# Kernel tuning notes

Hardware: AMD Instinct MI355X
Metric: run time of the kernel (lower is better)

Reference implementation:

```python
import jax, jax.numpy as jnp
import numpy as np

H, KV, D = 12, 2, 128        # q heads, kv heads, head_dim
HID = 1536
B, S = 4, 2048               # equal-length packed sequences
T = B * S
EPS = 1e-6
ROPE_THETA = 10000.0


def _rms_norm(x, w):
    # RMSNorm over last dim in fp32, as in Qwen3RMSNorm
    xf = x.astype(jnp.float32)
    var = jnp.mean(xf * xf, axis=-1, keepdims=True)
    return (w * (xf * jax.lax.rsqrt(var + EPS))).astype(x.dtype)


def _apply_rope(x, cos, sin):
    # x: [T, h, D]; cos/sin: [T, D/2] -> expand over heads
    half = cos.shape[-1]
    x1, x2 = x[..., :half], x[..., half:2 * half]
    c = cos[:, None, :]
    s = sin[:, None, :]
    return jnp.concatenate([x1 * c - x2 * s, x1 * s + x2 * c], axis=-1)


def setup_inputs() -> dict:
    key = jax.random.key(0)
    ks = jax.random.split(key, 8)
    hidden_states = jax.random.normal(ks[0], (T, HID), dtype=jnp.float32)
    # real RoPE tables over per-sequence positions
    inv_freq = 1.0 / (ROPE_THETA ** (np.arange(0, D, 2, dtype=np.float32) / D))  # [D/2]
    pos = np.tile(np.arange(S, dtype=np.float32), B)                              # [T]
    ang = pos[:, None] * inv_freq[None, :]
    cos = jnp.asarray(np.cos(ang), dtype=jnp.float32)
    sin = jnp.asarray(np.sin(ang), dtype=jnp.float32)
    sc = 0.02
    Wq = jax.random.normal(ks[1], (HID, H * D), dtype=jnp.float32) * sc
    Wk = jax.random.normal(ks[2], (HID, KV * D), dtype=jnp.float32) * sc
    Wv = jax.random.normal(ks[3], (HID, KV * D), dtype=jnp.float32) * sc
    Wo = jax.random.normal(ks[4], (H * D, HID), dtype=jnp.float32) * sc
    q_norm_w = jnp.ones((D,), dtype=jnp.float32)
    k_norm_w = jnp.ones((D,), dtype=jnp.float32)
    cu_seqlens = jnp.arange(B + 1, dtype=jnp.int32) * S
    return {"hidden_states": hidden_states, "cos": cos, "sin": sin,
            "Wq": Wq, "Wk": Wk, "Wv": Wv, "Wo": Wo,
            "q_norm_w": q_norm_w, "k_norm_w": k_norm_w,
            "cu_seqlens": cu_seqlens}


def reference(hidden_states, cos, sin, Wq, Wk, Wv, Wo, q_norm_w, k_norm_w, cu_seqlens):
    # QKV projections on packed tokens
    q = (hidden_states @ Wq).reshape(T, H, D)
    k = (hidden_states @ Wk).reshape(T, KV, D)
    v = (hidden_states @ Wv).reshape(T, KV, D)
    # Qwen3 per-head QK RMSNorm, then RoPE
    q = _apply_rope(_rms_norm(q, q_norm_w), cos, sin)
    k = _apply_rope(_rms_norm(k, k_norm_w), cos, sin)
    # equal-length sequences: unpack to [B, h, S, D] (block-diagonal varlen attn)
    qb = q.reshape(B, S, H, D).transpose(0, 2, 1, 3)
    kb = k.reshape(B, S, KV, D).transpose(0, 2, 1, 3)
    vb = v.reshape(B, S, KV, D).transpose(0, 2, 1, 3)
    # GQA: repeat kv heads
    rep = H // KV
    kb = jnp.repeat(kb, rep, axis=1)
    vb = jnp.repeat(vb, rep, axis=1)
    scale = D ** -0.5
    scores = jnp.einsum('bhqd,bhkd->bhqk', qb, kb) * scale
    causal = jnp.tril(jnp.ones((S, S), dtype=bool))
    scores = jnp.where(causal[None, None], scores, jnp.finfo(scores.dtype).min)
    attn = jax.nn.softmax(scores, axis=-1)
    out = jnp.einsum('bhqk,bhkd->bhqd', attn, vb)       # [B,H,S,D]
    out = out.transpose(0, 2, 1, 3).reshape(T, H * D)   # repack
    return out @ Wo
```

## Files before the change

### kernel.cpp

```cpp
#include <hip/hip_runtime.h>
#include <hip/hip_bf16.h>
#include <stdint.h>

#define H_   12
#define KV_  2
#define D_   128
#define HID_ 1536
#define B_   4
#define S_   2048
#define T_   (B_*S_)

typedef __attribute__((ext_vector_type(8))) short  bf16x8;
typedef __attribute__((ext_vector_type(4))) float  f32x4;

__device__ __forceinline__ ushort f2bf(float f) {
  union { float f; uint32_t u; } v; v.f = f;
  uint32_t u = v.u;
  return (ushort)((u + 0x7fffu + ((u >> 16) & 1u)) >> 16);
}
__device__ __forceinline__ float bf2f(ushort u) {
  union { uint32_t u; float f; } v; v.u = ((uint32_t)u) << 16;
  return v.f;
}
__device__ __forceinline__ uint32_t cvtpk_bf16(float lo, float hi) {
  uint32_t r;
  asm("v_cvt_pk_bf16_f32 %0, %1, %2" : "=v"(r) : "v"(lo), "v"(hi));
  return r;
}

__device__ __forceinline__ void gload_lds16(const void* g, void* l) {
  __builtin_amdgcn_global_load_lds(
      (const __attribute__((address_space(1))) uint32_t*)g,
      (__attribute__((address_space(3))) uint32_t*)l, 16, 0, 0);
}

__global__ __launch_bounds__(256) void cvt_f32_bf16(const float* __restrict__ in,
                                                    ushort* __restrict__ out, int n) {
  int i = (blockIdx.x * 256 + threadIdx.x) * 4;
  if (i + 3 < n) {
    float4 v = *(const float4*)&in[i];
    ushort4 o;
    o.x = f2bf(v.x); o.y = f2bf(v.y); o.z = f2bf(v.z); o.w = f2bf(v.w);
    *(ushort4*)&out[i] = o;
  }
}

__global__ __launch_bounds__(256) void transpose_cvt2(const float* __restrict__ W0,
                                                      ushort* __restrict__ Wt0,
                                                      const float* __restrict__ W1,
                                                      ushort* __restrict__ Wt1,
                                                      int K, int N) {
  __shared__ float tile[32][33];
  const float* W  = blockIdx.z ? W1  : W0;
  ushort*      Wt = blockIdx.z ? Wt1 : Wt0;
  int k0 = blockIdx.x * 32, n0 = blockIdx.y * 32;
  int tx = threadIdx.x & 31, ty = threadIdx.x >> 5;
#pragma unroll
  for (int i = 0; i < 32; i += 8)
    tile[ty + i][tx] = W[(long)(k0 + ty + i) * N + n0 + tx];
  __syncthreads();
#pragma unroll
  for (int i = 0; i < 32; i += 8)
    Wt[(long)(n0 + ty + i) * K + k0 + tx] = f2bf(tile[tx][ty + i]);
}

template <int OUT_F32>
__global__ __launch_bounds__(256, 2) void gemm_bt(const ushort* __restrict__ A,
                                                  const ushort* __restrict__ Bt,
                                                  void* __restrict__ Cv,
                                                  int M, int N, int K, int lda) {
  __shared__ ushort lA[128 * 32];
  __shared__ ushort lB[128 * 32];
  const int tid = threadIdx.x;
  const int lane = tid & 63, w = tid >> 6;
  const int wr = w >> 1, wc = w & 1;
  const int l15 = lane & 15, lh = lane >> 4;
  const long m0 = (long)blockIdx.x * 128, n0 = (long)blockIdx.y * 128;
  const ushort* Ab = A + m0 * lda;
  const ushort* Bb = Bt + n0 * K;
  const int sr = tid >> 2;
  const int sc = (tid & 3) * 8;
  const int ldsoff = w * 512;
  f32x4 acc[4][4] = {};

  for (int k0 = 0; k0 < K; k0 += 32) {
#pragma unroll
    for (int it = 0; it < 2; ++it) {
      gload_lds16(Ab + (long)(it * 64 + sr) * lda + k0 + sc, &lA[it * 2048 + ldsoff]);
      gload_lds16(Bb + (long)(it * 64 + sr) * K + k0 + sc, &lB[it * 2048 + ldsoff]);
    }
    __syncthreads();
    bf16x8 af[4], bfr[4];
    const int ra = (wr * 64 + l15) * 32 + lh * 8;
    const int rb = (wc * 64 + l15) * 32 + lh * 8;
#pragma unroll
    for (int i = 0; i < 4; ++i) {
      af[i]  = *(const bf16x8*)&lA[ra + i * 16 * 32];
      bfr[i] = *(const bf16x8*)&lB[rb + i * 16 * 32];
    }
#pragma unroll
    for (int i = 0; i < 4; ++i)
#pragma unroll
      for (int j = 0; j < 4; ++j)
        acc[i][j] = __builtin_amdgcn_mfma_f32_16x16x32_bf16(af[i], bfr[j], acc[i][j], 0, 0, 0);
    __syncthreads();
  }
#pragma unroll
  for (int i = 0; i < 4; ++i) {
#pragma unroll
    for (int q = 0; q < 4; ++q) {
      long row = m0 + wr * 64 + i * 16 + lh * 4 + q;
#pragma unroll
      for (int j = 0; j < 4; ++j) {
        long col = n0 + wc * 64 + j * 16 + l15;
        float v = acc[i][j][q];
        if (OUT_F32) ((float*)Cv)[row * N + col] = v;
        else         ((ushort*)Cv)[row * N + col] = f2bf(v);
      }
    }
  }
}

template <int OUT_F32>
__global__ __launch_bounds__(512) void gemm256(const ushort* __restrict__ A,
                                               const ushort* __restrict__ Bt,
                                               void* __restrict__ Cv,
                                               int M, int N, int K, int lda) {
  __shared__ ushort lA[2][256 * 64];
  __shared__ ushort lB[2][256 * 64];
  const int tid = threadIdx.x, lane = tid & 63;
  const int w = tid >> 6;
  const int l15 = lane & 15, lh = lane >> 4;
  const int wr = w >> 2, wc = w & 3;
  const long m0 = (long)blockIdx.x * 256, n0 = (long)blockIdx.y * 256;
  const ushort* Ab = A + m0 * lda;
  const ushort* Bb = Bt + n0 * K;
  const int swz = (l15 & 7) << 4;

  f32x4 acc[8][4] = {};
  const int NT = K / 64;

#define STAGE256(KT, PB) do {                                                      \
  const int k0s = (KT) * 64;                                                       \
  _Pragma("unroll") for (int it = 0; it < 4; ++it) {                               \
    int ch = it * 512 + tid; int r = ch >> 3, s = ch & 7;                          \
    int cb = it * 512 + (tid & 448);                                               \
    gload_lds16(Ab + (long)r * lda + k0s + ((s ^ (r & 7)) * 8), &lA[PB][cb * 8]);  \
  }                                                                                \
  _Pragma("unroll") for (int it = 0; it < 4; ++it) {                               \
    int ch = it * 512 + tid; int r = ch >> 3, s = ch & 7;                          \
    int cb = it * 512 + (tid & 448);                                               \
    gload_lds16(Bb + (long)r * K + k0s + ((s ^ (r & 7)) * 8), &lB[PB][cb * 8]);    \
  }                                                                                \
} while (0)

  STAGE256(0, 0);
  __syncthreads();
  int p = 0;
  for (int kt = 0; kt < NT; ++kt) {
    if (kt + 1 < NT) STAGE256(kt + 1, p ^ 1);
    const char* cA = (const char*)&lA[p][0];
    const char* cB = (const char*)&lB[p][0];
    bf16x8 bf[4][2];
#pragma unroll
    for (int fj = 0; fj < 4; ++fj)
#pragma unroll
      for (int kk = 0; kk < 2; ++kk)
        bf[fj][kk] = *(const bf16x8*)(cB + (wc * 64 + fj * 16 + l15) * 128 + ((kk * 64 + lh * 16) ^ swz));
    __builtin_amdgcn_s_setprio(1);
#pragma unroll
    for (int fi = 0; fi < 8; ++fi) {
      const int ra = (wr * 128 + fi * 16 + l15) * 128;
      bf16x8 af0 = *(const bf16x8*)(cA + ra + ((lh * 16) ^ swz));
      bf16x8 af1 = *(const bf16x8*)(cA + ra + ((64 + lh * 16) ^ swz));
#pragma unroll
      for (int fj = 0; fj < 4; ++fj) {
        acc[fi][fj] = __builtin_amdgcn_mfma_f32_16x16x32_bf16(af0, bf[fj][0], acc[fi][fj], 0, 0, 0);
        acc[fi][fj] = __builtin_amdgcn_mfma_f32_16x16x32_bf16(af1, bf[fj][1], acc[fi][fj], 0, 0, 0);
      }
    }
    __builtin_amdgcn_s_setprio(0);
    __syncthreads();
    p ^= 1;
  }
#undef STAGE256
#pragma unroll
  for (int fi = 0; fi < 8; ++fi) {
#pragma unroll
    for (int q = 0; q < 4; ++q) {
      long row = m0 + wr * 128 + fi * 16 + lh * 4 + q;
#pragma unroll
      for (int fj = 0; fj < 4; ++fj) {
        long col = n0 + wc * 64 + fj * 16 + l15;
        float v = acc[fi][fj][q];
        if (OUT_F32) ((float*)Cv)[row * N + col] = v;
        else         ((ushort*)Cv)[row * N + col] = f2bf(v);
      }
    }
  }
}

template <int NH>
__global__ __launch_bounds__(256) void normrope(const ushort* __restrict__ X,
                                                int xstride,
                                                const float* __restrict__ w,
                                                const float* __restrict__ cosb,
                                                const float* __restrict__ sinb,
                                                ushort* __restrict__ Y,
                                                float scale) {
  int wid = (int)((blockIdx.x * 256 + threadIdx.x) >> 6);
  int lane = threadIdx.x & 63;
  if (wid >= T_ * NH) return;
  int t = wid / NH, h = wid % NH;
  const ushort* xr = X + (long)t * xstride + h * 128;
  float x1 = bf2f(xr[lane]);
  float x2 = bf2f(xr[lane + 64]);
  float ss = x1 * x1 + x2 * x2;
#pragma unroll
  for (int off = 32; off; off >>= 1) ss += __shfl_xor(ss, off);
  float r = rsqrtf(ss * (1.0f / 128.0f) + 1e-6f);
  float y1 = x1 * r * w[lane] * scale;
  float y2 = x2 * r * w[lane + 64] * scale;
  float c = cosb[(long)t * 64 + lane], s = sinb[(long)t * 64 + lane];
  float o1 = y1 * c - y2 * s;
  float o2 = y1 * s + y2 * c;
  int b = t / S_, sq = t % S_;
  ushort* yr = Y + ((long)(b * NH + h) * S_ + sq) * 128;
  yr[lane]      = f2bf(o1);
  yr[lane + 64] = f2bf(o2);
}

__global__ __launch_bounds__(256) void vtrans(const ushort* __restrict__ V, int vstride, int voff,
                                              ushort* __restrict__ Vt) {
  __shared__ ushort tile[32][33];
  int s0 = blockIdx.x * 32, d0 = blockIdx.y * 32;
  int bk = blockIdx.z;
  int b = bk / KV_, g = bk % KV_;
  int tx = threadIdx.x & 31, ty = threadIdx.x >> 5;
#pragma unroll
  for (int i = 0; i < 32; i += 8)
    tile[ty + i][tx] = V[(long)(b * S_ + s0 + ty + i) * vstride + voff + g * 128 + d0 + tx];
  __syncthreads();
#pragma unroll
  for (int i = 0; i < 32; i += 8)
    Vt[(long)(bk * 128 + d0 + ty + i) * S_ + s0 + tx] = tile[tx][ty + i];
}

__global__ __launch_bounds__(256, 2) void attn(ushort* __restrict__ QKV,
                                               const ushort* __restrict__ Ka,
                                               const ushort* __restrict__ Vt,
                                               const float* __restrict__ qnw,
                                               const float* __restrict__ cosb,
                                               const float* __restrict__ sinb) {
  __shared__ ushort lK[64 * 128];
  __shared__ ushort lV[128 * 64];
  __shared__ ushort lP[4 * 32 * 32];
  const int tid = threadIdx.x, lane = tid & 63, w = tid >> 6;
  const int l15 = lane & 15, lh = lane >> 4;
  char* cK = (char*)lK;
  char* cV = (char*)lV;
  char* cP = (char*)lP + w * 2048;
  const int swzK = l15 << 4;
  const int swzV = (l15 & 7) << 4;
  const int swzP = (l15 & 3) << 4;
  const float SCL = 0.08838834764831845f * 1.44269504088896f;
  const float M0  = 17.0f;

  const int qt = 15 - (int)(blockIdx.x / 48);
  const int bh = blockIdx.x % 48;
  const int b = bh / H_, h = bh % H_, g = h / (H_ / KV_);
  const int q0 = qt * 128;
  const ushort* Kb = Ka + (long)(b * KV_ + g) * S_ * 128;
  const ushort* Vb = Vt + (long)(b * KV_ + g) * 128 * S_;

  bf16x8 qf[2][4];
#pragma unroll
  for (int m = 0; m < 2; ++m) {
    const long tt = (long)b * S_ + q0 + w * 32 + m * 16 + l15;
    const ushort* xr = QKV + tt * 2048 + h * 128;
    bf16x8 raw[4];
#pragma unroll
    for (int kd = 0; kd < 4; ++kd)
      raw[kd] = *(const bf16x8*)&xr[kd * 32 + lh * 8];
    float ss = 0.f;
#pragma unroll
    for (int kd = 0; kd < 4; ++kd)
#pragma unroll
      for (int e = 0; e < 8; ++e) {
        float v = bf2f((ushort)raw[kd][e]);
        ss += v * v;
      }
    ss += __shfl_xor(ss, 16);
    ss += __shfl_xor(ss, 32);
    const float rn = rsqrtf(ss * (1.0f / 128.0f) + 1e-6f) * SCL;
    const float* cR = cosb + tt * 64;
    const float* sR = sinb + tt * 64;
#pragma unroll
    for (int kp = 0; kp < 2; ++kp) {
      bf16x8 qlo, qhi;
#pragma unroll
      for (int e = 0; e < 8; ++e) {
        const int ci = kp * 32 + lh * 8 + e;
        float c = cR[ci], s = sR[ci];
        float y1 = bf2f((ushort)raw[kp][e])     * rn * qnw[ci];
        float y2 = bf2f((ushort)raw[kp + 2][e]) * rn * qnw[64 + ci];
        qlo[e] = (short)f2bf(y1 * c - y2 * s);
        qhi[e] = (short)f2bf(y1 * s + y2 * c);
      }
      qf[m][kp]     = qlo;
      qf[m][kp + 2] = qhi;
    }
  }

  f32x4 o[2][8] = {};
  float lr[2] = {0.f, 0.f};
  const int nt = 2 * qt + 2;

  bf16x8 kreg[4], vreg[4];
#define LDTILE(K0) do { \
  _Pragma("unroll") for (int it = 0; it < 4; ++it) \
    kreg[it] = *(const bf16x8*)&Kb[(long)((K0) + it * 16 + (tid >> 4)) * 128 + (tid & 15) * 8]; \
  _Pragma("unroll") for (int it = 0; it < 4; ++it) \
    vreg[it] = *(const bf16x8*)&Vb[(long)(it * 32 + (tid >> 3)) * S_ + (K0) + (tid & 7) * 8]; \
} while (0)

  LDTILE(0);
  for (int t = 0; t < nt; ++t) {
    const int k0 = t * 64;
    __syncthreads();
#pragma unroll
    for (int it = 0; it < 4; ++it) {
      int r = it * 16 + (tid >> 4);
      *(bf16x8*)(cK + r * 256 + (((tid & 15) * 16) ^ (((tid >> 4) & 15) << 4))) = kreg[it];
    }
#pragma unroll
    for (int it = 0; it < 4; ++it) {
      int r = it * 32 + (tid >> 3);
      *(bf16x8*)(cV + r * 128 + (((tid & 7) * 16) ^ ((r & 7) << 4))) = vreg[it];
    }
    __syncthreads();
    if (t + 1 < nt) LDTILE(k0 + 64);

    if (k0 <= q0 + w * 32 + 31) {
      f32x4 sfr[2][4] = {};
      __builtin_amdgcn_s_setprio(1);
#pragma unroll
      for (int kd = 0; kd < 4; ++kd) {
        bf16x8 kf[4];
#pragma unroll
        for (int n = 0; n < 4; ++n)
          kf[n] = *(const bf16x8*)(cK + (n * 16 + l15) * 256 + ((kd * 64 + lh * 16) ^ swzK));
#pragma unroll
        for (int m = 0; m < 2; ++m)
#pragma unroll
          for (int n = 0; n < 4; ++n)
            sfr[m][n] = __builtin_amdgcn_mfma_f32_16x16x32_bf16(kf[n], qf[m][kd], sfr[m][n], 0, 0, 0);
      }
      __builtin_amdgcn_s_setprio(0);
      const bool boundary = (k0 + 63 > q0 + w * 32);
      if (boundary) {
#pragma unroll
        for (int m = 0; m < 2; ++m) {
          const int rowm = q0 + w * 32 + m * 16 + l15;
#pragma unroll
          for (int n = 0; n < 4; ++n) {
            int kb = k0 + n * 16 + lh * 4;
#pragma unroll
            for (int qr = 0; qr < 4; ++qr)
              if (kb + qr > rowm) sfr[m][n][qr] = -INFINITY;
          }
        }
      }
#pragma unroll
      for (int m = 0; m < 2; ++m) {
#pragma unroll
        for (int n = 0; n < 4; ++n) {
          float p0 = exp2f(sfr[m][n][0] - M0);
          float p1 = exp2f(sfr[m][n][1] - M0);
          float p2 = exp2f(sfr[m][n][2] - M0);
          float p3 = exp2f(sfr[m][n][3] - M0);
          sfr[m][n][0] = p0; sfr[m][n][1] = p1; sfr[m][n][2] = p2; sfr[m][n][3] = p3;
          lr[m] += (p0 + p1) + (p2 + p3);
        }
      }
#pragma unroll
      for (int kf2 = 0; kf2 < 2; ++kf2) {
#pragma unroll
        for (int m = 0; m < 2; ++m)
#pragma unroll
          for (int nl = 0; nl < 2; ++nl) {
            const int n = kf2 * 2 + nl;
            uint2 pk;
            pk.x = cvtpk_bf16(sfr[m][n][0], sfr[m][n][1]);
            pk.y = cvtpk_bf16(sfr[m][n][2], sfr[m][n][3]);
            *(uint2*)(cP + (m * 16 + l15) * 64 + ((nl * 32 + lh * 8) ^ swzP)) = pk;
          }
        const int cb = (lh * 16) ^ swzP;
        bf16x8 pf0 = *(const bf16x8*)(cP + l15 * 64 + cb);
        bf16x8 pf1 = *(const bf16x8*)(cP + (16 + l15) * 64 + cb);
        const int cv = (kf2 * 64 + lh * 16);
        __builtin_amdgcn_s_setprio(1);
#pragma unroll
        for (int dblk = 0; dblk < 8; ++dblk) {
          bf16x8 vf = *(const bf16x8*)(cV + (dblk * 16 + l15) * 128 + (cv ^ swzV));
          o[0][dblk] = __builtin_amdgcn_mfma_f32_16x16x32_bf16(pf0, vf, o[0][dblk], 0, 0, 0);
          o[1][dblk] = __builtin_amdgcn_mfma_f32_16x16x32_bf16(pf1, vf, o[1][dblk], 0, 0, 0);
        }
        __builtin_amdgcn_s_setprio(0);
      }
    }
  }
#undef LDTILE
#pragma unroll
  for (int m = 0; m < 2; ++m) {
    lr[m] += __shfl_xor(lr[m], 16);
    lr[m] += __shfl_xor(lr[m], 32);
    float inv = 1.f / lr[m];
#pragma unroll
    for (int qr = 0; qr < 4; ++qr) {
      float iv = __shfl(inv, lh * 4 + qr);
      long trow = (long)b * S_ + q0 + w * 32 + m * 16 + lh * 4 + qr;
#pragma unroll
      for (int dblk = 0; dblk < 8; ++dblk)
        QKV[trow * 2048 + h * 128 + dblk * 16 + l15] = f2bf(o[m][dblk][qr] * iv);
    }
  }
}

extern "C" void kernel_launch(void* const* d_in, const int* in_sizes, int n_in,
                              void* d_out, int out_size, void* d_ws, size_t ws_size,
                              hipStream_t stream) {
  const float* hs   = (const float*)d_in[0];
  const float* cosb = (const float*)d_in[1];
  const float* sinb = (const float*)d_in[2];
  const float* Wq   = (const float*)d_in[3];
  const float* Wk   = (const float*)d_in[4];
  const float* Wv   = (const float*)d_in[5];
  const float* Wo   = (const float*)d_in[6];
  const float* qw   = (const float*)d_in[7];
  const float* kw   = (const float*)d_in[8];
  (void)in_sizes; (void)n_in; (void)out_size; (void)ws_size;

  char* ws = (char*)d_ws;
  size_t off = 0;
  auto alloc = [&](size_t bytes) {
    void* p = ws + off;
    off += (bytes + 255) & ~(size_t)255;
    return p;
  };
  ushort* Xb  = (ushort*)alloc((size_t)T_ * HID_ * 2);
  ushort* Wqt = (ushort*)alloc((size_t)HID_ * HID_ * 2);
  ushort* Wkt = (ushort*)alloc((size_t)256 * HID_ * 2);
  ushort* Wvt = (ushort*)alloc((size_t)256 * HID_ * 2);
  ushort* Wot = (ushort*)alloc((size_t)HID_ * HID_ * 2);
  ushort* qkv = (ushort*)alloc((size_t)T_ * 2048 * 2);
  ushort* ka  = (ushort*)alloc((size_t)T_ * 256 * 2);
  ushort* vt  = (ushort*)alloc((size_t)T_ * 256 * 2);

  cvt_f32_bf16<<<(T_ * HID_ / 4 + 255) / 256, 256, 0, stream>>>(hs, Xb, T_ * HID_);
  transpose_cvt2<<<dim3(HID_ / 32, HID_ / 32, 2), 256, 0, stream>>>(Wq, Wqt, Wo, Wot, HID_, HID_);
  transpose_cvt2<<<dim3(HID_ / 32, 256 / 32, 2), 256, 0, stream>>>(Wk, Wkt, Wv, Wvt, HID_, 256);

  gemm256<0><<<dim3(T_ / 256, 2048 / 256), 512, 0, stream>>>(Xb, Wqt, qkv, T_, 2048, HID_, HID_);

  normrope<KV_><<<(T_ * KV_ + 3) / 4, 256, 0, stream>>>(qkv + 1536, 2048, kw, cosb, sinb, ka, 1.0f);
  vtrans<<<dim3(S_ / 32, 128 / 32, B_ * KV_), 256, 0, stream>>>(qkv, 2048, 1792, vt);

  attn<<<768, 256, 0, stream>>>(qkv, ka, vt, qw, cosb, sinb);

  gemm_bt<1><<<dim3(T_ / 128, 1536 / 128), 256, 0, stream>>>(qkv, Wot, (float*)d_out, T_, 1536, HID_, 2048);
}
```

Before: 215.9 us.

## Split longest causal attention q-tiles across two blocks with finalize merge

The four longest query tiles (qt 12-15) are split along the KV dimension into two halves, each run by its own block, with a custom schedule order that interleaves split and unsplit tiles to balance load. Split blocks write unnormalized fp32 partial outputs and row sums to scratch (reusing the Xb buffer), and a new finalize kernel sums them and normalizes into QKV. This targets the tail imbalance of causal attention, at the cost of extra scratch traffic and one more kernel launch. The merge depends on the fixed max M0 shared across halves, so no max rescaling is needed.

Measured after the change: 225.0 us. +4.2%, slower.

```diff
diff --git a/kernel.cpp b/kernel.cpp
--- a/kernel.cpp
+++ b/kernel.cpp
@@ -246,12 +246,17 @@
     Vt[(long)(bk * 128 + d0 + ty + i) * S_ + s0 + tx] = tile[tx][ty + i];
 }
 
+__device__ const signed char DQT[20] = {11,10,9,8,7,15,15,14,14,6,13,13,12,12,5,4,3,2,1,0};
+__device__ const signed char DHF[20] = {-1,-1,-1,-1,-1, 0, 1, 0, 1,-1, 0, 1, 0, 1,-1,-1,-1,-1,-1,-1};
+
 __global__ __launch_bounds__(256, 2) void attn(ushort* __restrict__ QKV,
                                                const ushort* __restrict__ Ka,
                                                const ushort* __restrict__ Vt,
                                                const float* __restrict__ qnw,
                                                const float* __restrict__ cosb,
-                                               const float* __restrict__ sinb) {
+                                               const float* __restrict__ sinb,
+                                               float* __restrict__ scO,
+                                               float* __restrict__ scL) {
   __shared__ ushort lK[64 * 128];
   __shared__ ushort lV[128 * 64];
   __shared__ ushort lP[4 * 32 * 32];
@@ -266,10 +271,15 @@
   const float SCL = 0.08838834764831845f * 1.44269504088896f;
   const float M0  = 17.0f;
 
-  const int qt = 15 - (int)(blockIdx.x / 48);
+  const int u  = (int)(blockIdx.x / 48);
   const int bh = blockIdx.x % 48;
+  const int qt = DQT[u];
+  const int hf = DHF[u];
   const int b = bh / H_, h = bh % H_, g = h / (H_ / KV_);
   const int q0 = qt * 128;
+  const int t0 = (hf == 1) ? (qt + 1) : 0;
+  const int t1 = (hf == 0) ? (qt + 1) : (2 * qt + 2);
+  const bool split = (hf >= 0);
   const ushort* Kb = Ka + (long)(b * KV_ + g) * S_ * 128;
   const ushort* Vb = Vt + (long)(b * KV_ + g) * 128 * S_;
 
@@ -314,7 +324,6 @@
 
   f32x4 o[2][8] = {};
   float lr[2] = {0.f, 0.f};
-  const int nt = 2 * qt + 2;
 
   bf16x8 kreg[4], vreg[4];
 #define LDTILE(K0) do { \
@@ -324,8 +333,8 @@
     vreg[it] = *(const bf16x8*)&Vb[(long)(it * 32 + (tid >> 3)) * S_ + (K0) + (tid & 7) * 8]; \
 } while (0)
 
-  LDTILE(0);
-  for (int t = 0; t < nt; ++t) {
+  LDTILE(t0 * 64);
+  for (int t = t0; t < t1; ++t) {
     const int k0 = t * 64;
     __syncthreads();
 #pragma unroll
@@ -339,7 +348,7 @@
       *(bf16x8*)(cV + r * 128 + (((tid & 7) * 16) ^ ((r & 7) << 4))) = vreg[it];
     }
     __syncthreads();
-    if (t + 1 < nt) LDTILE(k0 + 64);
+    if (t + 1 < t1) LDTILE((t + 1) * 64);
 
     if (k0 <= q0 + w * 32 + 31) {
       f32x4 sfr[2][4] = {};
@@ -415,15 +424,63 @@
   for (int m = 0; m < 2; ++m) {
     lr[m] += __shfl_xor(lr[m], 16);
     lr[m] += __shfl_xor(lr[m], 32);
-    float inv = 1.f / lr[m];
-#pragma unroll
-    for (int qr = 0; qr < 4; ++qr) {
-      float iv = __shfl(inv, lh * 4 + qr);
-      long trow = (long)b * S_ + q0 + w * 32 + m * 16 + lh * 4 + qr;
-#pragma unroll
-      for (int dblk = 0; dblk < 8; ++dblk)
-        QKV[trow * 2048 + h * 128 + dblk * 16 + l15] = f2bf(o[m][dblk][qr] * iv);
-    }
+  }
+  if (!split) {
+#pragma unroll
+    for (int m = 0; m < 2; ++m) {
+      float inv = 1.f / lr[m];
+#pragma unroll
+      for (int qr = 0; qr < 4; ++qr) {
+        float iv = __shfl(inv, lh * 4 + qr);
+        long trow = (long)b * S_ + q0 + w * 32 + m * 16 + lh * 4 + qr;
+#pragma unroll
+        for (int dblk = 0; dblk < 8; ++dblk)
+          QKV[trow * 2048 + h * 128 + dblk * 16 + l15] = f2bf(o[m][dblk][qr] * iv);
+      }
+    }
+  } else {
+    const int slot = (((qt - 12) * 48 + bh) * 2 + hf);
+    float* So = scO + (long)slot * 16384;
+#pragma unroll
+    for (int m = 0; m < 2; ++m) {
+      if (lh == 0) scL[slot * 128 + w * 32 + m * 16 + l15] = lr[m];
+#pragma unroll
+      for (int qr = 0; qr < 4; ++qr) {
+        int row = w * 32 + m * 16 + lh * 4 + qr;
+#pragma unroll
+        for (int dblk = 0; dblk < 8; ++dblk)
+          So[row * 128 + dblk * 16 + l15] = o[m][dblk][qr];
+      }
+    }
+  }
+}
+
+__global__ __launch_bounds__(256) void attn_finalize(const float* __restrict__ scO,
+                                                     const float* __restrict__ scL,
+                                                     ushort* __restrict__ QKV) {
+  const int u = blockIdx.x;
+  const int qti = u / 48, bh = u % 48;
+  const int qt = 12 + qti;
+  const int b = bh / H_, h = bh % H_;
+  const int tid = threadIdx.x;
+  const int slot0 = ((qti * 48 + bh) * 2);
+  const float* O0 = scO + (long)slot0 * 16384;
+  const float* O1 = O0 + 16384;
+  const float* L0 = scL + slot0 * 128;
+  const float* L1 = L0 + 128;
+  const int c2 = (tid & 63) * 2;
+  const int rg = tid >> 6;
+#pragma unroll
+  for (int i = 0; i < 32; ++i) {
+    const int row = rg + i * 4;
+    float inv = 1.f / (L0[row] + L1[row]);
+    float2 a = *(const float2*)&O0[row * 128 + c2];
+    float2 bb = *(const float2*)&O1[row * 128 + c2];
+    ushort2 ov;
+    ov.x = f2bf((a.x + bb.x) * inv);
+    ov.y = f2bf((a.y + bb.y) * inv);
+    long trow = (long)b * S_ + qt * 128 + row;
+    *(ushort2*)&QKV[trow * 2048 + h * 128 + c2] = ov;
   }
 }
 
@@ -456,6 +513,8 @@
   ushort* qkv = (ushort*)alloc((size_t)T_ * 2048 * 2);
   ushort* ka  = (ushort*)alloc((size_t)T_ * 256 * 2);
   ushort* vt  = (ushort*)alloc((size_t)T_ * 256 * 2);
+  float*  scL = (float*)alloc((size_t)384 * 128 * 4);
+  float*  scO = (float*)Xb;
 
   cvt_f32_bf16<<<(T_ * HID_ / 4 + 255) / 256, 256, 0, stream>>>(hs, Xb, T_ * HID_);
   transpose_cvt2<<<dim3(HID_ / 32, HID_ / 32, 2), 256, 0, stream>>>(Wq, Wqt, Wo, Wot, HID_, HID_);
@@ -466,7 +525,8 @@
   normrope<KV_><<<(T_ * KV_ + 3) / 4, 256, 0, stream>>>(qkv + 1536, 2048, kw, cosb, sinb, ka, 1.0f);
   vtrans<<<dim3(S_ / 32, 128 / 32, B_ * KV_), 256, 0, stream>>>(qkv, 2048, 1792, vt);
 
-  attn<<<768, 256, 0, stream>>>(qkv, ka, vt, qw, cosb, sinb);
+  attn<<<960, 256, 0, stream>>>(qkv, ka, vt, qw, cosb, sinb, scO, scL);
+  attn_finalize<<<192, 256, 0, stream>>>(scO, scL, qkv);
 
   gemm_bt<1><<<dim3(T_ / 128, 1536 / 128), 256, 0, stream>>>(qkv, Wot, (float*)d_out, T_, 1536, HID_, 2048);
 }
```
